# Kernel tuning notes

Measured on AMD Instinct MI355X. Metric: run time of the kernel, lower is better.

## Reference

```python
import jax, jax.numpy as jnp
import numpy as np

# FP4 E2M1 lookup: sign bit in nibble bit 3, values {0,.5,1,1.5,2,3,4,6}
FP4_VALUES = jnp.array([0.0, 0.5, 1.0, 1.5, 2.0, 3.0, 4.0, 6.0,
                        -0.0, -0.5, -1.0, -1.5, -2.0, -3.0, -4.0, -6.0],
                       dtype=jnp.float32)
BLOCK = 32  # MX block size: one E8M0 scale per 32 elements along K
E8M0_BIAS = 127.0


def _dequant_mxfp4(packed, scales):
    """packed: [R, K//2] int bytes (two fp4 nibbles each, low nibble first).
    scales: [R, K//32] float32 biased E8M0 exponents. Returns [R, K] float32."""
    lo = packed & 0xF
    hi = (packed >> 4) & 0xF
    idx = jnp.stack([lo, hi], axis=-1).reshape(packed.shape[0], -1)  # [R, K]
    vals = FP4_VALUES[idx]                                           # [R, K]
    R, K = vals.shape
    scale = jnp.exp2(scales - E8M0_BIAS)                             # [R, K//32]
    vals = vals.reshape(R, K // BLOCK, BLOCK) * scale[..., None]
    return vals.reshape(R, K)


def setup_inputs() -> dict:
    key = jax.random.key(0)
    k1, k2, k3, k4 = jax.random.split(key, 4)
    M = N = 4096
    K = 4096
    a = jax.random.randint(k1, (M, K // 2), 0, 256, dtype=jnp.int32)
    b = jax.random.randint(k2, (N, K // 2), 0, 256, dtype=jnp.int32)
    scales_a = jax.random.randint(k3, (M, K // BLOCK), 120, 132).astype(jnp.float32)
    scales_b = jax.random.randint(k4, (N, K // BLOCK), 120, 132).astype(jnp.float32)
    return {"a": a, "b": b, "scales_a": scales_a, "scales_b": scales_b}


def reference(a, b, scales_a, scales_b):
    a_f = _dequant_mxfp4(a, scales_a)          # [M, K]
    b_f = _dequant_mxfp4(b, scales_b)          # [N, K]
    return jnp.einsum('mk,nk->mn', a_f, b_f)   # [M, N]
```

## Files before the change

### kernel.cpp

```cpp
#include <hip/hip_runtime.h>
#include <hip/hip_bf16.h>
#include <stdint.h>

typedef __attribute__((ext_vector_type(4))) int          i32x4;
typedef __attribute__((ext_vector_type(8))) int          i32x8;
typedef __attribute__((ext_vector_type(4))) float        f32x4;
typedef __attribute__((ext_vector_type(4))) unsigned int u32x4;

#define MDIM   4096
#define NDIM   4096
#define KBYTES 2048
#define NKBLK  128

#define BM   128
#define BN   128
#define BKB  128
#define KT   (KBYTES / BKB)

#define BARF()  asm volatile("s_barrier" ::: "memory")
#define LGKM0() asm volatile("s_waitcnt lgkmcnt(0)" ::: "memory")
#define VM0()   asm volatile("s_waitcnt vmcnt(0)" ::: "memory")

__global__ void repack_all(const int* __restrict__ a, const int* __restrict__ b,
                           const float* __restrict__ sa, const float* __restrict__ sb,
                           u32x4* __restrict__ ap, u32x4* __restrict__ bp,
                           uint8_t* __restrict__ satT, uint8_t* __restrict__ sbtT) {
  const int t = blockIdx.x * blockDim.x + threadIdx.x;
  {
    const size_t i = (size_t)t;
    uint32_t r[4], s[4];
#pragma unroll
    for (int q = 0; q < 4; ++q) {
      i32x4 va = *(const i32x4*)(a + i * 16 + q * 4);
      r[q] = (uint32_t)(va.x & 255) | ((uint32_t)(va.y & 255) << 8) |
             ((uint32_t)(va.z & 255) << 16) | ((uint32_t)(va.w & 255) << 24);
      i32x4 vb = *(const i32x4*)(b + i * 16 + q * 4);
      s[q] = (uint32_t)(vb.x & 255) | ((uint32_t)(vb.y & 255) << 8) |
             ((uint32_t)(vb.z & 255) << 16) | ((uint32_t)(vb.w & 255) << 24);
    }
    u32x4 rv = {r[0], r[1], r[2], r[3]};
    u32x4 sv = {s[0], s[1], s[2], s[3]};
    ap[i] = rv;
    bp[i] = sv;
  }
  {
    const int m = t >> 7, kb = t & 127;
    const int o = ((kb >> 3) * 32 + (m >> 7)) * 1024 + (kb & 7) * 128 + (m & 15) * 8
                  + ((m >> 4) & 7);
    satT[o] = (uint8_t)(int)sa[t];
    sbtT[o] = (uint8_t)(int)sb[t];
  }
}

__device__ __forceinline__ i32x8 frag8(i32x4 v) {
  i32x8 r = {v.x, v.y, v.z, v.w, 0, 0, 0, 0};
  return r;
}

__global__ __launch_bounds__(256, 4) void mxfp4_gemm(
    const uint8_t* __restrict__ ap, const uint8_t* __restrict__ bp,
    const uint8_t* __restrict__ satT, const uint8_t* __restrict__ sbtT,
    float* __restrict__ out) {
  __shared__ __align__(16) uint8_t lds[34816];

  const int tid  = threadIdx.x;
  const int lane = tid & 63;
  const int w    = tid >> 6;
  const int wrow = w >> 1;
  const int wcol = w & 1;
  const int g    = lane >> 4;
  const int l15  = lane & 15;
  const int lx   = lane & 7;

  const int wgid = (blockIdx.x & 7) * 128 + (blockIdx.x >> 3);
  const int bx = wgid & 31;
  const int by = wgid >> 5;

  const uint8_t* aBase = ap + (size_t)(by * BM) * KBYTES;
  const uint8_t* bBase = bp + (size_t)(bx * BN) * KBYTES;
  uint8_t* const lA  = lds;
  uint8_t* const lB  = lds + 16384;
  uint8_t* const scb = lds + 32768;

  const int srow  = lane >> 3;
  const int sslot = (lane & 7) ^ srow;
  const int soff  = srow * KBYTES + sslot * 16;
  const int arow0 = w * 32;

#define STAGE(ktX)                                                                        \
  do {                                                                                    \
    _Pragma("unroll")                                                                     \
    for (int c = 0; c < 4; ++c) {                                                         \
      const int r0 = arow0 + c * 8;                                                       \
      __builtin_amdgcn_global_load_lds(                                                   \
          (__attribute__((address_space(1))) void*)(aBase + (size_t)r0 * KBYTES + (ktX) * BKB + soff), \
          (__attribute__((address_space(3))) void*)(lA + r0 * 128), 16, 0, 0);            \
      __builtin_amdgcn_global_load_lds(                                                   \
          (__attribute__((address_space(1))) void*)(bBase + (size_t)r0 * KBYTES + (ktX) * BKB + soff), \
          (__attribute__((address_space(3))) void*)(lB + r0 * 128), 16, 0, 0);            \
    }                                                                                     \
    __builtin_amdgcn_global_load_lds(                                                     \
        (__attribute__((address_space(1))) void*)(satT + ((size_t)(ktX) * 32 + by) * 1024 + lane * 16), \
        (__attribute__((address_space(3))) void*)(scb + lane * 16), 16, 0, 0);            \
    __builtin_amdgcn_global_load_lds(                                                     \
        (__attribute__((address_space(1))) void*)(sbtT + ((size_t)(ktX) * 32 + bx) * 1024 + lane * 16), \
        (__attribute__((address_space(3))) void*)(scb + 1024 + lane * 16), 16, 0, 0);     \
  } while (0)

  f32x4 acc[4][4] = {};
  i32x4 af[4], bf[4];

  STAGE(0);

  for (int kt = 0; kt < KT; ++kt) {
    VM0();
    BARF();

    const uint32_t sAk0 = *(const uint32_t*)(scb + (0 + g) * 128 + l15 * 8 + wrow * 4);
    const uint32_t sAk1 = *(const uint32_t*)(scb + (4 + g) * 128 + l15 * 8 + wrow * 4);
    const uint32_t sBk0 = *(const uint32_t*)(scb + 1024 + (0 + g) * 128 + l15 * 8 + wcol * 4);
    const uint32_t sBk1 = *(const uint32_t*)(scb + 1024 + (4 + g) * 128 + l15 * 8 + wcol * 4);

    {
      const int slotx = ((0 + g) ^ lx) * 16;
#pragma unroll
      for (int ns = 0; ns < 4; ++ns)
        bf[ns] = *(const i32x4*)(lB + (wcol * 64 + ns * 16 + l15) * 128 + slotx);
#pragma unroll
      for (int ms = 0; ms < 4; ++ms)
        af[ms] = *(const i32x4*)(lA + (wrow * 64 + ms * 16 + l15) * 128 + slotx);
      __builtin_amdgcn_s_setprio(1);
#pragma unroll
      for (int ms = 0; ms < 4; ++ms) {
        const int sa = (int)((sAk0 >> (ms * 8)) & 0xffu);
#pragma unroll
        for (int ns = 0; ns < 4; ++ns)
          acc[ms][ns] = __builtin_amdgcn_mfma_scale_f32_16x16x128_f8f6f4(
              frag8(af[ms]), frag8(bf[ns]), acc[ms][ns], 4, 4,
              0, sa, 0, (int)((sBk0 >> (ns * 8)) & 0xffu));
      }
      __builtin_amdgcn_s_setprio(0);
    }
    {
      const int slotx = ((4 + g) ^ lx) * 16;
#pragma unroll
      for (int ns = 0; ns < 4; ++ns)
        bf[ns] = *(const i32x4*)(lB + (wcol * 64 + ns * 16 + l15) * 128 + slotx);
#pragma unroll
      for (int ms = 0; ms < 4; ++ms)
        af[ms] = *(const i32x4*)(lA + (wrow * 64 + ms * 16 + l15) * 128 + slotx);
      __builtin_amdgcn_s_setprio(1);
#pragma unroll
      for (int ms = 0; ms < 4; ++ms) {
        const int sa = (int)((sAk1 >> (ms * 8)) & 0xffu);
#pragma unroll
        for (int ns = 0; ns < 4; ++ns)
          acc[ms][ns] = __builtin_amdgcn_mfma_scale_f32_16x16x128_f8f6f4(
              frag8(af[ms]), frag8(bf[ns]), acc[ms][ns], 4, 4,
              0, sa, 0, (int)((sBk1 >> (ns * 8)) & 0xffu));
      }
      __builtin_amdgcn_s_setprio(0);
    }

    LGKM0();
    BARF();
    if (kt + 1 < KT) STAGE(kt + 1);
  }

  float* ob = out + (size_t)(by * BM + wrow * 64) * NDIM + bx * BN + wcol * 64;
#pragma unroll
  for (int ms = 0; ms < 4; ++ms)
#pragma unroll
    for (int ns = 0; ns < 4; ++ns) {
#pragma unroll
      for (int r = 0; r < 4; ++r)
        ob[(size_t)(ms * 16 + g * 4 + r) * NDIM + ns * 16 + l15] = acc[ms][ns][r];
    }
#undef STAGE
}

extern "C" void kernel_launch(void* const* d_in, const int* in_sizes, int n_in,
                              void* d_out, int out_size, void* d_ws, size_t ws_size,
                              hipStream_t stream) {
  (void)in_sizes; (void)n_in; (void)out_size; (void)ws_size;
  const int*   a  = (const int*)d_in[0];
  const int*   b  = (const int*)d_in[1];
  const float* sa = (const float*)d_in[2];
  const float* sb = (const float*)d_in[3];
  float* out = (float*)d_out;

  uint8_t* ws = (uint8_t*)d_ws;
  u32x4*   ap   = (u32x4*)ws;
  u32x4*   bp   = (u32x4*)(ws + (8u << 20));
  uint8_t* satT = ws + (16u << 20);
  uint8_t* sbtT = ws + (16u << 20) + (512u << 10);

  repack_all<<<2048, 256, 0, stream>>>(a, b, sa, sb, ap, bp, satT, sbtT);

  dim3 grid(32 * 32);
  mxfp4_gemm<<<grid, 256, 0, stream>>>((const uint8_t*)ap, (const uint8_t*)bp,
                                       satT, sbtT, out);
}
```

Before: 69.75 us.

## Split scale repack into coalesced LDS-transpose kernel and use MFMA scale op-select

```diff
diff --git a/kernel.cpp b/kernel.cpp
--- a/kernel.cpp
+++ b/kernel.cpp
@@ -21,35 +21,45 @@
 #define LGKM0() asm volatile("s_waitcnt lgkmcnt(0)" ::: "memory")
 #define VM0()   asm volatile("s_waitcnt vmcnt(0)" ::: "memory")
 
-__global__ void repack_all(const int* __restrict__ a, const int* __restrict__ b,
-                           const float* __restrict__ sa, const float* __restrict__ sb,
-                           u32x4* __restrict__ ap, u32x4* __restrict__ bp,
-                           uint8_t* __restrict__ satT, uint8_t* __restrict__ sbtT) {
-  const int t = blockIdx.x * blockDim.x + threadIdx.x;
-  {
-    const size_t i = (size_t)t;
-    uint32_t r[4], s[4];
-#pragma unroll
-    for (int q = 0; q < 4; ++q) {
-      i32x4 va = *(const i32x4*)(a + i * 16 + q * 4);
-      r[q] = (uint32_t)(va.x & 255) | ((uint32_t)(va.y & 255) << 8) |
-             ((uint32_t)(va.z & 255) << 16) | ((uint32_t)(va.w & 255) << 24);
-      i32x4 vb = *(const i32x4*)(b + i * 16 + q * 4);
-      s[q] = (uint32_t)(vb.x & 255) | ((uint32_t)(vb.y & 255) << 8) |
-             ((uint32_t)(vb.z & 255) << 16) | ((uint32_t)(vb.w & 255) << 24);
-    }
-    u32x4 rv = {r[0], r[1], r[2], r[3]};
-    u32x4 sv = {s[0], s[1], s[2], s[3]};
-    ap[i] = rv;
-    bp[i] = sv;
+__global__ void repack_bytes(const int* __restrict__ a, const int* __restrict__ b,
+                             u32x4* __restrict__ ap, u32x4* __restrict__ bp) {
+  const size_t i = (size_t)(blockIdx.x * blockDim.x + threadIdx.x);
+  uint32_t r[4], s[4];
+#pragma unroll
+  for (int q = 0; q < 4; ++q) {
+    i32x4 va = *(const i32x4*)(a + i * 16 + q * 4);
+    r[q] = (uint32_t)(va.x & 255) | ((uint32_t)(va.y & 255) << 8) |
+           ((uint32_t)(va.z & 255) << 16) | ((uint32_t)(va.w & 255) << 24);
+    i32x4 vb = *(const i32x4*)(b + i * 16 + q * 4);
+    s[q] = (uint32_t)(vb.x & 255) | ((uint32_t)(vb.y & 255) << 8) |
+           ((uint32_t)(vb.z & 255) << 16) | ((uint32_t)(vb.w & 255) << 24);
   }
-  {
-    const int m = t >> 7, kb = t & 127;
-    const int o = ((kb >> 3) * 32 + (m >> 7)) * 1024 + (kb & 7) * 128 + (m & 15) * 8
-                  + ((m >> 4) & 7);
-    satT[o] = (uint8_t)(int)sa[t];
-    sbtT[o] = (uint8_t)(int)sb[t];
+  u32x4 rv = {r[0], r[1], r[2], r[3]};
+  u32x4 sv = {s[0], s[1], s[2], s[3]};
+  ap[i] = rv;
+  bp[i] = sv;
+}
+
+__global__ void repack_scales(const float* __restrict__ sa, const float* __restrict__ sb,
+                              uint8_t* __restrict__ satT, uint8_t* __restrict__ sbtT) {
+  __shared__ uint8_t ls[2][1024];
+  const int kt = blockIdx.x & 15, rb = blockIdx.x >> 4;
+  const int t  = threadIdx.x;
+  const int mm = t >> 1;
+  const int j0 = (t & 1) * 4;
+  const size_t src = (size_t)(rb * 128 + mm) * 128 + kt * 8 + j0;
+  const f32x4 va = *(const f32x4*)(sa + src);
+  const f32x4 vb = *(const f32x4*)(sb + src);
+#pragma unroll
+  for (int q = 0; q < 4; ++q) {
+    const int o = (j0 + q) * 128 + (mm & 15) * 8 + ((mm >> 4) & 7);
+    ls[0][o] = (uint8_t)(int)va[q];
+    ls[1][o] = (uint8_t)(int)vb[q];
   }
+  __syncthreads();
+  const size_t dst = ((size_t)kt * 32 + rb) * 1024 + t * 4;
+  *(uint32_t*)(satT + dst) = *(const uint32_t*)&ls[0][t * 4];
+  *(uint32_t*)(sbtT + dst) = *(const uint32_t*)&ls[1][t * 4];
 }
 
 __device__ __forceinline__ i32x8 frag8(i32x4 v) {
@@ -107,6 +117,12 @@
         (__attribute__((address_space(3))) void*)(scb + 1024 + lane * 16), 16, 0, 0);     \
   } while (0)
 
+#define MM(msL, nsL, sAv, sBv)                                                            \
+  acc[msL][nsL] = __builtin_amdgcn_mfma_scale_f32_16x16x128_f8f6f4(                       \
+      frag8(af[msL]), frag8(bf[nsL]), acc[msL][nsL], 4, 4, msL, (int)(sAv), nsL, (int)(sBv))
+#define MMROW(msL, sAv, sBv)                                                              \
+  MM(msL, 0, sAv, sBv); MM(msL, 1, sAv, sBv); MM(msL, 2, sAv, sBv); MM(msL, 3, sAv, sBv)
+
   f32x4 acc[4][4] = {};
   i32x4 af[4], bf[4];
 
@@ -130,15 +146,10 @@
       for (int ms = 0; ms < 4; ++ms)
         af[ms] = *(const i32x4*)(lA + (wrow * 64 + ms * 16 + l15) * 128 + slotx);
       __builtin_amdgcn_s_setprio(1);
-#pragma unroll
-      for (int ms = 0; ms < 4; ++ms) {
-        const int sa = (int)((sAk0 >> (ms * 8)) & 0xffu);
-#pragma unroll
-        for (int ns = 0; ns < 4; ++ns)
-          acc[ms][ns] = __builtin_amdgcn_mfma_scale_f32_16x16x128_f8f6f4(
-              frag8(af[ms]), frag8(bf[ns]), acc[ms][ns], 4, 4,
-              0, sa, 0, (int)((sBk0 >> (ns * 8)) & 0xffu));
-      }
+      MMROW(0, sAk0, sBk0);
+      MMROW(1, sAk0, sBk0);
+      MMROW(2, sAk0, sBk0);
+      MMROW(3, sAk0, sBk0);
       __builtin_amdgcn_s_setprio(0);
     }
     {
@@ -150,15 +161,10 @@
       for (int ms = 0; ms < 4; ++ms)
         af[ms] = *(const i32x4*)(lA + (wrow * 64 + ms * 16 + l15) * 128 + slotx);
       __builtin_amdgcn_s_setprio(1);
-#pragma unroll
-      for (int ms = 0; ms < 4; ++ms) {
-        const int sa = (int)((sAk1 >> (ms * 8)) & 0xffu);
-#pragma unroll
-        for (int ns = 0; ns < 4; ++ns)
-          acc[ms][ns] = __builtin_amdgcn_mfma_scale_f32_16x16x128_f8f6f4(
-              frag8(af[ms]), frag8(bf[ns]), acc[ms][ns], 4, 4,
-              0, sa, 0, (int)((sBk1 >> (ns * 8)) & 0xffu));
-      }
+      MMROW(0, sAk1, sBk1);
+      MMROW(1, sAk1, sBk1);
+      MMROW(2, sAk1, sBk1);
+      MMROW(3, sAk1, sBk1);
       __builtin_amdgcn_s_setprio(0);
     }
 
@@ -177,6 +183,8 @@
         ob[(size_t)(ms * 16 + g * 4 + r) * NDIM + ns * 16 + l15] = acc[ms][ns][r];
     }
 #undef STAGE
+#undef MM
+#undef MMROW
 }
 
 extern "C" void kernel_launch(void* const* d_in, const int* in_sizes, int n_in,
@@ -195,7 +203,8 @@
   uint8_t* satT = ws + (16u << 20);
   uint8_t* sbtT = ws + (16u << 20) + (512u << 10);
 
-  repack_all<<<2048, 256, 0, stream>>>(a, b, sa, sb, ap, bp, satT, sbtT);
+  repack_bytes<<<2048, 256, 0, stream>>>(a, b, ap, bp);
+  repack_scales<<<512, 256, 0, stream>>>(sa, sb, satT, sbtT);
 
   dim3 grid(32 * 32);
   mxfp4_gemm<<<grid, 256, 0, stream>>>((const uint8_t*)ap, (const uint8_t*)bp,
```

After: 69.78 us. No clear change (+0.0%).
